# Kernel tuning notes

Hardware: AMD Instinct MI355X
Metric: run time of the kernel (lower is better)

Reference implementation:

```python
import jax, jax.numpy as jnp
import numpy as np

B, H, S, DK = 2, 16, 2048, 64

def setup_inputs() -> dict:
    key = jax.random.key(0)
    kq, kk, kv = jax.random.split(key, 3)
    shape = (B, H, S, DK)
    return {
        "multi_head_q": jax.random.normal(kq, shape, dtype=jnp.float32),
        "multi_head_k": jax.random.normal(kk, shape, dtype=jnp.float32),
        "multi_head_v": jax.random.normal(kv, shape, dtype=jnp.float32),
    }

def reference(multi_head_q, multi_head_k, multi_head_v):
    d_k = multi_head_q.shape[-1]
    scale = 1.0 / jnp.sqrt(jnp.asarray(d_k, dtype=multi_head_q.dtype))
    # scores: [B, H, S, S]
    scores = jnp.einsum("bhqd,bhkd->bhqk", multi_head_q, multi_head_k) * scale
    attn = jax.nn.softmax(scores, axis=-1)
    # z: [B, H, S, DK]
    z = jnp.einsum("bhqk,bhkd->bhqd", attn, multi_head_v)
    # transpose heads to [B, S, H, DK] then merge -> [B, S, H*DK]
    b, h, s, d = z.shape
    return jnp.swapaxes(z, 1, 2).reshape(b, s, h * d)
```

## Files before the change

kernel.cpp:

```cpp
#include <hip/hip_runtime.h>
#include <cmath>


#define S_LEN   2048
#define D_HEAD  64
#define NHEADS  16
#define NBH     32
#define TQ      128
#define TK      64
#define NTILE   (S_LEN / TK)
#define LDSTR   72
#define TILE_SH 4096

typedef short bfrag8 __attribute__((ext_vector_type(8)));
typedef float f32x4  __attribute__((ext_vector_type(4)));
typedef int   i32x2  __attribute__((ext_vector_type(2)));
typedef int   i32x4  __attribute__((ext_vector_type(4)));

static __device__ __forceinline__ short f2bf(float f) {
  unsigned int u = __builtin_bit_cast(unsigned int, f);
  u = (u + 0x7fffu + ((u >> 16) & 1u)) >> 16;
  return (short)(unsigned short)u;
}

static __device__ __forceinline__ int pk2bf(float a, float b) {
#if __has_builtin(__builtin_amdgcn_cvt_pk_bf16_f32)
  typedef __bf16 bf16x2 __attribute__((ext_vector_type(2)));
  bf16x2 r = __builtin_amdgcn_cvt_pk_bf16_f32(a, b);
  return __builtin_bit_cast(int, r);
#else
  return (int)(unsigned short)f2bf(a) | ((int)(unsigned short)f2bf(b) << 16);
#endif
}

static __device__ __forceinline__ float fexp2(float x) {
#if __has_builtin(__builtin_amdgcn_exp2f)
  return __builtin_amdgcn_exp2f(x);
#else
  return exp2f(x);
#endif
}

static __device__ __forceinline__ void gload_lds16(const short* g, short* l) {
  __builtin_amdgcn_global_load_lds(
      (const __attribute__((address_space(1))) void*)g,
      (__attribute__((address_space(3))) void*)l, 16, 0, 0);
}

__global__ __launch_bounds__(256)
void fa_prep(const float* __restrict__ K, const float* __restrict__ V,
             short* __restrict__ Kt, short* __restrict__ Vt) {
  __shared__ float fl[64][65];

  const int tid = threadIdx.x;
  const int id  = blockIdx.x;
  const int xcd = id & 7;
  const int s   = id >> 3;
  const int bh  = xcd * 4 + (s >> 5);
  const int t   = s & 31;

  const size_t ibase = ((size_t)bh * S_LEN + t * 64) * D_HEAD;
  short* kt = Kt + (size_t)(bh * NTILE + t) * TILE_SH;
  short* vt = Vt + (size_t)(bh * NTILE + t) * TILE_SH;

#pragma unroll
  for (int p = 0; p < 2; ++p) {
    int idx = p * 256 + tid;
    int key = idx >> 3, c = idx & 7;
    const float* src = K + ibase + key * 64 + c * 8;
    float4 a = *(const float4*)src;
    float4 b = *(const float4*)(src + 4);
    i32x4 w;
    w[0] = pk2bf(a.x, a.y); w[1] = pk2bf(a.z, a.w);
    w[2] = pk2bf(b.x, b.y); w[3] = pk2bf(b.z, b.w);
    *(i32x4*)(kt + key * 64 + ((c ^ (key & 7)) * 8)) = w;
  }

#pragma unroll
  for (int i = 0; i < 4; ++i) {
    int e = (i * 256 + tid) * 4;
    int row = e >> 6, col = e & 63;
    float4 v = *(const float4*)(V + ibase + (size_t)row * 64 + col);
    fl[col + 0][row] = v.x;
    fl[col + 1][row] = v.y;
    fl[col + 2][row] = v.z;
    fl[col + 3][row] = v.w;
  }
  __syncthreads();
#pragma unroll
  for (int p = 0; p < 2; ++p) {
    int idx = p * 256 + tid;
    int d = idx >> 3, ck = idx & 7;
    const float* row = &fl[d][ck * 8];
    i32x4 w;
    w[0] = pk2bf(row[0], row[1]); w[1] = pk2bf(row[2], row[3]);
    w[2] = pk2bf(row[4], row[5]); w[3] = pk2bf(row[6], row[7]);
    *(i32x4*)(vt + d * 64 + ((ck ^ (d & 7)) * 8)) = w;
  }
}

__global__ __launch_bounds__(256, 2)
void fa_fwd3(const float* __restrict__ Q, const short* __restrict__ Kt,
             const short* __restrict__ Vt, float* __restrict__ Out) {
  __shared__ short Ksb[2][TILE_SH];
  __shared__ short Vsb[2][TILE_SH];
  __shared__ short Ps [TQ * LDSTR];

  const int tid  = threadIdx.x;
  const int wid  = tid >> 6;
  const int lane = tid & 63;
  const int quad = lane >> 4;
  const int r    = lane & 15;
  const int rk   = r & 7;
  const int qb   = 32 * wid;

  const int id   = blockIdx.x;
  const int xcd  = id & 7;
  const int slot = id >> 3;
  const int bh   = xcd * 4 + (slot >> 4);
  const int q0   = (slot & 15) * TQ;

  const float qscale = 0.125f * 1.44269504088896340736f;

  const float* Qg = Q + (size_t)bh * S_LEN * D_HEAD;
  bfrag8 qf[2][2];
#pragma unroll
  for (int nt = 0; nt < 2; ++nt)
#pragma unroll
    for (int ks = 0; ks < 2; ++ks) {
      const float* qp = Qg + (size_t)(q0 + qb + 16 * nt + r) * D_HEAD + 32 * ks + 8 * quad;
      float4 a = *(const float4*)qp;
      float4 b = *(const float4*)(qp + 4);
      i32x4 w;
      w[0] = pk2bf(a.x * qscale, a.y * qscale);
      w[1] = pk2bf(a.z * qscale, a.w * qscale);
      w[2] = pk2bf(b.x * qscale, b.y * qscale);
      w[3] = pk2bf(b.z * qscale, b.w * qscale);
      qf[nt][ks] = __builtin_bit_cast(bfrag8, w);
    }

  const short* ktb = Kt + (size_t)bh * NTILE * TILE_SH;
  const short* vtb = Vt + (size_t)bh * NTILE * TILE_SH;

  auto stage = [&](int b, int t) {
    const short* ks = ktb + (size_t)t * TILE_SH;
    const short* vs = vtb + (size_t)t * TILE_SH;
#pragma unroll
    for (int n = 0; n < 2; ++n) {
      int ch = (wid * 2 + n) * 512;
      gload_lds16(ks + ch + lane * 8, &Ksb[b][ch]);
      gload_lds16(vs + ch + lane * 8, &Vsb[b][ch]);
    }
  };

  f32x4 acc[4][2];
#pragma unroll
  for (int mt = 0; mt < 4; ++mt)
#pragma unroll
    for (int nt = 0; nt < 2; ++nt)
      acc[mt][nt] = (f32x4){0.f, 0.f, 0.f, 0.f};

  float lrun[2] = {0.f, 0.f};

  auto compute = [&](const short* ksb, const short* vsb) {
    f32x4 st[4][2];
#pragma unroll
    for (int mt = 0; mt < 4; ++mt)
#pragma unroll
      for (int nt = 0; nt < 2; ++nt)
        st[mt][nt] = (f32x4){0.f, 0.f, 0.f, 0.f};

#pragma unroll
    for (int ks = 0; ks < 2; ++ks) {
      bfrag8 af[4];
#pragma unroll
      for (int mt = 0; mt < 4; ++mt)
        af[mt] = *(const bfrag8*)&ksb[(r + 16 * mt) * 64 + (((quad + 4 * ks) ^ rk) * 8)];
#pragma unroll
      for (int mt = 0; mt < 4; ++mt)
#pragma unroll
        for (int nt = 0; nt < 2; ++nt)
          st[mt][nt] = __builtin_amdgcn_mfma_f32_16x16x32_bf16(af[mt], qf[nt][ks], st[mt][nt], 0, 0, 0);
    }

#pragma unroll
    for (int nt = 0; nt < 2; ++nt) {
      float ssum = 0.f;
#pragma unroll
      for (int mt = 0; mt < 4; ++mt) {
        float p0 = fexp2(st[mt][nt][0]);
        float p1 = fexp2(st[mt][nt][1]);
        float p2 = fexp2(st[mt][nt][2]);
        float p3 = fexp2(st[mt][nt][3]);
        ssum += (p0 + p1) + (p2 + p3);
        i32x2 w;
        w[0] = pk2bf(p0, p1);
        w[1] = pk2bf(p2, p3);
        *(i32x2*)&Ps[(qb + 16 * nt + r) * LDSTR + 16 * mt + 4 * quad] = w;
      }
      lrun[nt] += ssum;
    }

#pragma unroll
    for (int ks = 0; ks < 2; ++ks) {
      bfrag8 av[4], bp[2];
#pragma unroll
      for (int mt = 0; mt < 4; ++mt)
        av[mt] = *(const bfrag8*)&vsb[(r + 16 * mt) * 64 + (((quad + 4 * ks) ^ rk) * 8)];
#pragma unroll
      for (int nt = 0; nt < 2; ++nt)
        bp[nt] = *(const bfrag8*)&Ps[(qb + 16 * nt + r) * LDSTR + quad * 8 + 32 * ks];
#pragma unroll
      for (int mt = 0; mt < 4; ++mt)
#pragma unroll
        for (int nt = 0; nt < 2; ++nt)
          acc[mt][nt] = __builtin_amdgcn_mfma_f32_16x16x32_bf16(av[mt][0] == av[mt][0] ? av[mt] : av[mt], bp[nt], acc[mt][nt], 0, 0, 0);
    }
  };

  stage(0, 0);
  for (int t = 0; t < NTILE; t += 2) {
    __syncthreads();
    stage(1, t + 1);
    compute(Ksb[0], Vsb[0]);
    __syncthreads();
    if (t + 2 < NTILE) stage(0, t + 2);
    compute(Ksb[1], Vsb[1]);
  }

  const int bb = bh >> 4, hh = bh & 15;
#pragma unroll
  for (int nt = 0; nt < 2; ++nt) {
    float l = lrun[nt];
    l += __shfl_xor(l, 16);
    l += __shfl_xor(l, 32);
    float inv = 1.0f / l;
    int qg = q0 + qb + 16 * nt + r;
    float* op = Out + ((size_t)bb * S_LEN + qg) * (NHEADS * D_HEAD) + hh * D_HEAD;
#pragma unroll
    for (int mt = 0; mt < 4; ++mt) {
      float4 o;
      o.x = acc[mt][nt][0] * inv; o.y = acc[mt][nt][1] * inv;
      o.z = acc[mt][nt][2] * inv; o.w = acc[mt][nt][3] * inv;
      *(float4*)(op + 16 * mt + 4 * quad) = o;
    }
  }
}

__global__ __launch_bounds__(256, 2)
void fa_fwd(const float* __restrict__ Q, const float* __restrict__ K,
            const float* __restrict__ V, float* __restrict__ Out) {
  __shared__ short Ks [2][TK * LDSTR];
  __shared__ short VsT[2][D_HEAD * LDSTR];
  __shared__ short Psf[TQ * LDSTR];

  const int tid  = threadIdx.x;
  const int wid  = tid >> 6;
  const int lane = tid & 63;
  const int quad = lane >> 4;
  const int r    = lane & 15;
  const int qb   = 32 * wid;

  const int bh = blockIdx.y;
  const int q0 = blockIdx.x * TQ;

  const float* Qg = Q + (size_t)bh * S_LEN * D_HEAD;
  const float* Kg = K + (size_t)bh * S_LEN * D_HEAD;
  const float* Vg = V + (size_t)bh * S_LEN * D_HEAD;

  const float qscale = 0.125f * 1.44269504088896340736f;

  bfrag8 qf[2][2];
#pragma unroll
  for (int nt = 0; nt < 2; ++nt)
#pragma unroll
    for (int ks = 0; ks < 2; ++ks) {
      const float* qp = Qg + (size_t)(q0 + qb + 16 * nt + r) * D_HEAD + 32 * ks + 8 * quad;
      float4 a = *(const float4*)qp;
      float4 b = *(const float4*)(qp + 4);
      i32x4 w;
      w[0] = pk2bf(a.x * qscale, a.y * qscale);
      w[1] = pk2bf(a.z * qscale, a.w * qscale);
      w[2] = pk2bf(b.x * qscale, b.y * qscale);
      w[3] = pk2bf(b.z * qscale, b.w * qscale);
      qf[nt][ks] = __builtin_bit_cast(bfrag8, w);
    }

  float4 kpre[4];
  float  vpre[16];

  auto load_tile = [&](int k0) {
#pragma unroll
    for (int i = 0; i < 4; ++i) {
      int e = (i * 256 + tid) * 4;
      kpre[i] = *(const float4*)(Kg + (size_t)(k0 + (e >> 6)) * D_HEAD + (e & 63));
    }
    const float* vpp = Vg + (size_t)(k0 + wid * 16) * D_HEAD + lane;
#pragma unroll
    for (int j = 0; j < 16; ++j) vpre[j] = vpp[(size_t)j * D_HEAD];
  };

  auto store_tile = [&](short* ksb, short* vsb) {
#pragma unroll
    for (int i = 0; i < 4; ++i) {
      int e = (i * 256 + tid) * 4;
      i32x2 w;
      w[0] = pk2bf(kpre[i].x, kpre[i].y);
      w[1] = pk2bf(kpre[i].z, kpre[i].w);
      *(i32x2*)&ksb[(e >> 6) * LDSTR + (e & 63)] = w;
    }
    i32x4 w0, w1;
#pragma unroll
    for (int j = 0; j < 4; ++j) w0[j] = pk2bf(vpre[2 * j],     vpre[2 * j + 1]);
#pragma unroll
    for (int j = 0; j < 4; ++j) w1[j] = pk2bf(vpre[8 + 2 * j], vpre[9 + 2 * j]);
    *(i32x4*)&vsb[lane * LDSTR + wid * 16]     = w0;
    *(i32x4*)&vsb[lane * LDSTR + wid * 16 + 8] = w1;
  };

  f32x4 acc[4][2];
#pragma unroll
  for (int mt = 0; mt < 4; ++mt)
#pragma unroll
    for (int nt = 0; nt < 2; ++nt)
      acc[mt][nt] = (f32x4){0.f, 0.f, 0.f, 0.f};

  float lrun[2] = {0.f, 0.f};

  auto compute = [&](const short* ksb, const short* vsb) {
    f32x4 st[4][2];
#pragma unroll
    for (int mt = 0; mt < 4; ++mt)
#pragma unroll
      for (int nt = 0; nt < 2; ++nt)
        st[mt][nt] = (f32x4){0.f, 0.f, 0.f, 0.f};
#pragma unroll
    for (int ks = 0; ks < 2; ++ks) {
      bfrag8 af[4];
#pragma unroll
      for (int mt = 0; mt < 4; ++mt)
        af[mt] = *(const bfrag8*)&ksb[(r + 16 * mt) * LDSTR + quad * 8 + 32 * ks];
#pragma unroll
      for (int mt = 0; mt < 4; ++mt)
#pragma unroll
        for (int nt = 0; nt < 2; ++nt)
          st[mt][nt] = __builtin_amdgcn_mfma_f32_16x16x32_bf16(af[mt], qf[nt][ks], st[mt][nt], 0, 0, 0);
    }
#pragma unroll
    for (int nt = 0; nt < 2; ++nt) {
      float ssum = 0.f;
#pragma unroll
      for (int mt = 0; mt < 4; ++mt) {
        float p0 = fexp2(st[mt][nt][0]);
        float p1 = fexp2(st[mt][nt][1]);
        float p2 = fexp2(st[mt][nt][2]);
        float p3 = fexp2(st[mt][nt][3]);
        ssum += (p0 + p1) + (p2 + p3);
        i32x2 w;
        w[0] = pk2bf(p0, p1);
        w[1] = pk2bf(p2, p3);
        *(i32x2*)&Psf[(qb + 16 * nt + r) * LDSTR + 16 * mt + 4 * quad] = w;
      }
      lrun[nt] += ssum;
    }
#pragma unroll
    for (int ks = 0; ks < 2; ++ks) {
      bfrag8 av[4], bp[2];
#pragma unroll
      for (int mt = 0; mt < 4; ++mt)
        av[mt] = *(const bfrag8*)&vsb[(r + 16 * mt) * LDSTR + quad * 8 + 32 * ks];
#pragma unroll
      for (int nt = 0; nt < 2; ++nt)
        bp[nt] = *(const bfrag8*)&Psf[(qb + 16 * nt + r) * LDSTR + quad * 8 + 32 * ks];
#pragma unroll
      for (int mt = 0; mt < 4; ++mt)
#pragma unroll
        for (int nt = 0; nt < 2; ++nt)
          acc[mt][nt] = __builtin_amdgcn_mfma_f32_16x16x32_bf16(av[mt], bp[nt], acc[mt][nt], 0, 0, 0);
    }
  };

  load_tile(0);
  store_tile(Ks[0], VsT[0]);
  load_tile(TK);

  for (int it = 0; it < NTILE; it += 2) {
    __syncthreads();
    compute(Ks[0], VsT[0]);
    store_tile(Ks[1], VsT[1]);
    if (it + 2 < NTILE) load_tile((it + 2) * TK);
    __syncthreads();
    compute(Ks[1], VsT[1]);
    if (it + 2 < NTILE) {
      store_tile(Ks[0], VsT[0]);
      if (it + 3 < NTILE) load_tile((it + 3) * TK);
    }
  }

  const int bb = bh >> 4, hh = bh & 15;
#pragma unroll
  for (int nt = 0; nt < 2; ++nt) {
    float l = lrun[nt];
    l += __shfl_xor(l, 16);
    l += __shfl_xor(l, 32);
    float inv = 1.0f / l;
    int qg = q0 + qb + 16 * nt + r;
    float* op = Out + ((size_t)bb * S_LEN + qg) * (NHEADS * D_HEAD) + hh * D_HEAD;
#pragma unroll
    for (int mt = 0; mt < 4; ++mt) {
      float4 o;
      o.x = acc[mt][nt][0] * inv; o.y = acc[mt][nt][1] * inv;
      o.z = acc[mt][nt][2] * inv; o.w = acc[mt][nt][3] * inv;
      *(float4*)(op + 16 * mt + 4 * quad) = o;
    }
  }
}

extern "C" void kernel_launch(void* const* d_in, const int* in_sizes, int n_in,
                              void* d_out, int out_size, void* d_ws, size_t ws_size,
                              hipStream_t stream) {
  const float* Q = (const float*)d_in[0];
  const float* K = (const float*)d_in[1];
  const float* V = (const float*)d_in[2];
  float* O = (float*)d_out;

  const size_t telems = (size_t)NBH * NTILE * TILE_SH;
  const size_t need   = 2 * telems * sizeof(short);

  if (ws_size >= need) {
    short* Kt = (short*)d_ws;
    short* Vt = Kt + telems;
    fa_prep<<<dim3(NBH * NTILE), 256, 0, stream>>>(K, V, Kt, Vt);
    fa_fwd3<<<dim3(512), 256, 0, stream>>>(Q, Kt, Vt, O);
  } else {
    dim3 grid(S_LEN / TQ, NBH);
    fa_fwd<<<grid, 256, 0, stream>>>(Q, K, V, O);
  }
}
```

Before: 146.5 us.

## Use 32x32x16 MFMA with register-resident P via permlane32 swap

Rewrites the attention main kernel to use 32x32x16 bf16 MFMAs, with each wave owning 32 queries and 128-thread blocks of 64 queries (1024 blocks). The P matrix is repacked in registers with v_permlane32_swap instead of going through an LDS round-trip, removing the Ps buffer and its write/read plus the LDS traffic. It adds s_setprio around the MFMA sections and splits the prep kernel into separate K and V blocks for more parallelism. The bf16 conversion helpers switch to a plain __bf16 cast. The risks are fewer waves per block to hide latency, and more K/V tile staging per block because each block now covers fewer queries.

```diff
diff --git a/kernel.cpp b/kernel.cpp
--- a/kernel.cpp
+++ b/kernel.cpp
@@ -14,23 +14,18 @@
 
 typedef short bfrag8 __attribute__((ext_vector_type(8)));
 typedef float f32x4  __attribute__((ext_vector_type(4)));
+typedef float f32x16 __attribute__((ext_vector_type(16)));
 typedef int   i32x2  __attribute__((ext_vector_type(2)));
 typedef int   i32x4  __attribute__((ext_vector_type(4)));
 
 static __device__ __forceinline__ short f2bf(float f) {
-  unsigned int u = __builtin_bit_cast(unsigned int, f);
-  u = (u + 0x7fffu + ((u >> 16) & 1u)) >> 16;
-  return (short)(unsigned short)u;
+  return (short)__builtin_bit_cast(unsigned short, (__bf16)f);
 }
 
 static __device__ __forceinline__ int pk2bf(float a, float b) {
-#if __has_builtin(__builtin_amdgcn_cvt_pk_bf16_f32)
-  typedef __bf16 bf16x2 __attribute__((ext_vector_type(2)));
-  bf16x2 r = __builtin_amdgcn_cvt_pk_bf16_f32(a, b);
-  return __builtin_bit_cast(int, r);
-#else
-  return (int)(unsigned short)f2bf(a) | ((int)(unsigned short)f2bf(b) << 16);
-#endif
+  unsigned short lo = __builtin_bit_cast(unsigned short, (__bf16)a);
+  unsigned short hi = __builtin_bit_cast(unsigned short, (__bf16)b);
+  return (int)lo | ((int)hi << 16);
 }
 
 static __device__ __forceinline__ float fexp2(float x) {
@@ -53,91 +48,92 @@
   __shared__ float fl[64][65];
 
   const int tid = threadIdx.x;
-  const int id  = blockIdx.x;
+  int id = blockIdx.x;
+  const bool isV = id >= NBH * NTILE;
+  if (isV) id -= NBH * NTILE;
   const int xcd = id & 7;
   const int s   = id >> 3;
   const int bh  = xcd * 4 + (s >> 5);
   const int t   = s & 31;
 
   const size_t ibase = ((size_t)bh * S_LEN + t * 64) * D_HEAD;
-  short* kt = Kt + (size_t)(bh * NTILE + t) * TILE_SH;
-  short* vt = Vt + (size_t)(bh * NTILE + t) * TILE_SH;
-
-#pragma unroll
-  for (int p = 0; p < 2; ++p) {
-    int idx = p * 256 + tid;
-    int key = idx >> 3, c = idx & 7;
-    const float* src = K + ibase + key * 64 + c * 8;
-    float4 a = *(const float4*)src;
-    float4 b = *(const float4*)(src + 4);
-    i32x4 w;
-    w[0] = pk2bf(a.x, a.y); w[1] = pk2bf(a.z, a.w);
-    w[2] = pk2bf(b.x, b.y); w[3] = pk2bf(b.z, b.w);
-    *(i32x4*)(kt + key * 64 + ((c ^ (key & 7)) * 8)) = w;
-  }
-
-#pragma unroll
-  for (int i = 0; i < 4; ++i) {
-    int e = (i * 256 + tid) * 4;
-    int row = e >> 6, col = e & 63;
-    float4 v = *(const float4*)(V + ibase + (size_t)row * 64 + col);
-    fl[col + 0][row] = v.x;
-    fl[col + 1][row] = v.y;
-    fl[col + 2][row] = v.z;
-    fl[col + 3][row] = v.w;
-  }
-  __syncthreads();
-#pragma unroll
-  for (int p = 0; p < 2; ++p) {
-    int idx = p * 256 + tid;
-    int d = idx >> 3, ck = idx & 7;
-    const float* row = &fl[d][ck * 8];
-    i32x4 w;
-    w[0] = pk2bf(row[0], row[1]); w[1] = pk2bf(row[2], row[3]);
-    w[2] = pk2bf(row[4], row[5]); w[3] = pk2bf(row[6], row[7]);
-    *(i32x4*)(vt + d * 64 + ((ck ^ (d & 7)) * 8)) = w;
-  }
-}
-
-__global__ __launch_bounds__(256, 2)
+
+  if (!isV) {
+    short* kt = Kt + (size_t)(bh * NTILE + t) * TILE_SH;
+#pragma unroll
+    for (int p = 0; p < 2; ++p) {
+      int idx = p * 256 + tid;
+      int key = idx >> 3, c = idx & 7;
+      const float* src = K + ibase + key * 64 + c * 8;
+      float4 a = *(const float4*)src;
+      float4 b = *(const float4*)(src + 4);
+      i32x4 w;
+      w[0] = pk2bf(a.x, a.y); w[1] = pk2bf(a.z, a.w);
+      w[2] = pk2bf(b.x, b.y); w[3] = pk2bf(b.z, b.w);
+      *(i32x4*)(kt + key * 64 + ((c ^ (key & 7)) * 8)) = w;
+    }
+  } else {
+    short* vt = Vt + (size_t)(bh * NTILE + t) * TILE_SH;
+#pragma unroll
+    for (int i = 0; i < 4; ++i) {
+      int e = (i * 256 + tid) * 4;
+      int row = e >> 6, col = e & 63;
+      float4 v = *(const float4*)(V + ibase + (size_t)row * 64 + col);
+      fl[col + 0][row] = v.x;
+      fl[col + 1][row] = v.y;
+      fl[col + 2][row] = v.z;
+      fl[col + 3][row] = v.w;
+    }
+    __syncthreads();
+#pragma unroll
+    for (int p = 0; p < 2; ++p) {
+      int idx = p * 256 + tid;
+      int d = idx >> 3, ck = idx & 7;
+      const float* row = &fl[d][ck * 8];
+      i32x4 w;
+      w[0] = pk2bf(row[0], row[1]); w[1] = pk2bf(row[2], row[3]);
+      w[2] = pk2bf(row[4], row[5]); w[3] = pk2bf(row[6], row[7]);
+      *(i32x4*)(vt + d * 64 + ((ck ^ (d & 7)) * 8)) = w;
+    }
+  }
+}
+
+__global__ __launch_bounds__(128, 2)
 void fa_fwd3(const float* __restrict__ Q, const short* __restrict__ Kt,
              const short* __restrict__ Vt, float* __restrict__ Out) {
   __shared__ short Ksb[2][TILE_SH];
   __shared__ short Vsb[2][TILE_SH];
-  __shared__ short Ps [TQ * LDSTR];
 
   const int tid  = threadIdx.x;
   const int wid  = tid >> 6;
   const int lane = tid & 63;
-  const int quad = lane >> 4;
-  const int r    = lane & 15;
-  const int rk   = r & 7;
+  const int h    = lane >> 5;
+  const int c    = lane & 31;
+  const int c7   = c & 7;
   const int qb   = 32 * wid;
 
   const int id   = blockIdx.x;
   const int xcd  = id & 7;
   const int slot = id >> 3;
-  const int bh   = xcd * 4 + (slot >> 4);
-  const int q0   = (slot & 15) * TQ;
+  const int bh   = xcd * 4 + (slot >> 5);
+  const int q0   = (slot & 31) * 64;
 
   const float qscale = 0.125f * 1.44269504088896340736f;
 
-  const float* Qg = Q + (size_t)bh * S_LEN * D_HEAD;
-  bfrag8 qf[2][2];
-#pragma unroll
-  for (int nt = 0; nt < 2; ++nt)
-#pragma unroll
-    for (int ks = 0; ks < 2; ++ks) {
-      const float* qp = Qg + (size_t)(q0 + qb + 16 * nt + r) * D_HEAD + 32 * ks + 8 * quad;
-      float4 a = *(const float4*)qp;
-      float4 b = *(const float4*)(qp + 4);
-      i32x4 w;
-      w[0] = pk2bf(a.x * qscale, a.y * qscale);
-      w[1] = pk2bf(a.z * qscale, a.w * qscale);
-      w[2] = pk2bf(b.x * qscale, b.y * qscale);
-      w[3] = pk2bf(b.z * qscale, b.w * qscale);
-      qf[nt][ks] = __builtin_bit_cast(bfrag8, w);
-    }
+  const float* Qg = Q + ((size_t)bh * S_LEN + (q0 + qb + c)) * D_HEAD;
+  bfrag8 qf[4];
+#pragma unroll
+  for (int sl = 0; sl < 4; ++sl) {
+    const float* qp = Qg + 16 * sl + 8 * h;
+    float4 a = *(const float4*)qp;
+    float4 b = *(const float4*)(qp + 4);
+    i32x4 w;
+    w[0] = pk2bf(a.x * qscale, a.y * qscale);
+    w[1] = pk2bf(a.z * qscale, a.w * qscale);
+    w[2] = pk2bf(b.x * qscale, b.y * qscale);
+    w[3] = pk2bf(b.z * qscale, b.w * qscale);
+    qf[sl] = __builtin_bit_cast(bfrag8, w);
+  }
 
   const short* ktb = Kt + (size_t)bh * NTILE * TILE_SH;
   const short* vtb = Vt + (size_t)bh * NTILE * TILE_SH;
@@ -146,76 +142,75 @@
     const short* ks = ktb + (size_t)t * TILE_SH;
     const short* vs = vtb + (size_t)t * TILE_SH;
 #pragma unroll
-    for (int n = 0; n < 2; ++n) {
-      int ch = (wid * 2 + n) * 512;
+    for (int n = 0; n < 4; ++n) {
+      int ch = (wid * 4 + n) * 512;
       gload_lds16(ks + ch + lane * 8, &Ksb[b][ch]);
       gload_lds16(vs + ch + lane * 8, &Vsb[b][ch]);
     }
   };
 
-  f32x4 acc[4][2];
-#pragma unroll
-  for (int mt = 0; mt < 4; ++mt)
-#pragma unroll
-    for (int nt = 0; nt < 2; ++nt)
-      acc[mt][nt] = (f32x4){0.f, 0.f, 0.f, 0.f};
-
-  float lrun[2] = {0.f, 0.f};
+  f32x16 acc[2];
+#pragma unroll
+  for (int m = 0; m < 2; ++m)
+#pragma unroll
+    for (int i = 0; i < 16; ++i) acc[m][i] = 0.f;
+
+  float lrun = 0.f;
 
   auto compute = [&](const short* ksb, const short* vsb) {
-    f32x4 st[4][2];
-#pragma unroll
-    for (int mt = 0; mt < 4; ++mt)
-#pragma unroll
-      for (int nt = 0; nt < 2; ++nt)
-        st[mt][nt] = (f32x4){0.f, 0.f, 0.f, 0.f};
-
-#pragma unroll
-    for (int ks = 0; ks < 2; ++ks) {
-      bfrag8 af[4];
-#pragma unroll
-      for (int mt = 0; mt < 4; ++mt)
-        af[mt] = *(const bfrag8*)&ksb[(r + 16 * mt) * 64 + (((quad + 4 * ks) ^ rk) * 8)];
-#pragma unroll
-      for (int mt = 0; mt < 4; ++mt)
-#pragma unroll
-        for (int nt = 0; nt < 2; ++nt)
-          st[mt][nt] = __builtin_amdgcn_mfma_f32_16x16x32_bf16(af[mt], qf[nt][ks], st[mt][nt], 0, 0, 0);
-    }
-
-#pragma unroll
-    for (int nt = 0; nt < 2; ++nt) {
-      float ssum = 0.f;
-#pragma unroll
-      for (int mt = 0; mt < 4; ++mt) {
-        float p0 = fexp2(st[mt][nt][0]);
-        float p1 = fexp2(st[mt][nt][1]);
-        float p2 = fexp2(st[mt][nt][2]);
-        float p3 = fexp2(st[mt][nt][3]);
-        ssum += (p0 + p1) + (p2 + p3);
-        i32x2 w;
-        w[0] = pk2bf(p0, p1);
-        w[1] = pk2bf(p2, p3);
-        *(i32x2*)&Ps[(qb + 16 * nt + r) * LDSTR + 16 * mt + 4 * quad] = w;
+    f32x16 st[2];
+#pragma unroll
+    for (int m = 0; m < 2; ++m)
+#pragma unroll
+      for (int i = 0; i < 16; ++i) st[m][i] = 0.f;
+
+    __builtin_amdgcn_s_setprio(1);
+#pragma unroll
+    for (int m2 = 0; m2 < 2; ++m2)
+#pragma unroll
+      for (int sl = 0; sl < 4; ++sl) {
+        bfrag8 af = *(const bfrag8*)
+            &ksb[(32 * m2 + c) * 64 + (((2 * sl + h) ^ c7) * 8)];
+        st[m2] = __builtin_amdgcn_mfma_f32_32x32x16_bf16(af, qf[sl], st[m2], 0, 0, 0);
       }
-      lrun[nt] += ssum;
-    }
-
-#pragma unroll
-    for (int ks = 0; ks < 2; ++ks) {
-      bfrag8 av[4], bp[2];
-#pragma unroll
-      for (int mt = 0; mt < 4; ++mt)
-        av[mt] = *(const bfrag8*)&vsb[(r + 16 * mt) * 64 + (((quad + 4 * ks) ^ rk) * 8)];
-#pragma unroll
-      for (int nt = 0; nt < 2; ++nt)
-        bp[nt] = *(const bfrag8*)&Ps[(qb + 16 * nt + r) * LDSTR + quad * 8 + 32 * ks];
-#pragma unroll
-      for (int mt = 0; mt < 4; ++mt)
-#pragma unroll
-        for (int nt = 0; nt < 2; ++nt)
-          acc[mt][nt] = __builtin_amdgcn_mfma_f32_16x16x32_bf16(av[mt][0] == av[mt][0] ? av[mt] : av[mt], bp[nt], acc[mt][nt], 0, 0, 0);
-    }
+    __builtin_amdgcn_s_setprio(0);
+
+    float ls = 0.f;
+#pragma unroll
+    for (int m2 = 0; m2 < 2; ++m2)
+#pragma unroll
+      for (int i = 0; i < 16; ++i) {
+        st[m2][i] = fexp2(st[m2][i]);
+        ls += st[m2][i];
+      }
+    lrun += ls;
+
+    bfrag8 pf[4];
+#pragma unroll
+    for (int m2 = 0; m2 < 2; ++m2)
+#pragma unroll
+      for (int hf = 0; hf < 2; ++hf) {
+        const int b0 = 8 * hf;
+        int w0 = pk2bf(st[m2][b0 + 0], st[m2][b0 + 1]);
+        int w1 = pk2bf(st[m2][b0 + 2], st[m2][b0 + 3]);
+        int w2 = pk2bf(st[m2][b0 + 4], st[m2][b0 + 5]);
+        int w3 = pk2bf(st[m2][b0 + 6], st[m2][b0 + 7]);
+        asm("v_permlane32_swap_b32 %0, %1" : "+v"(w0), "+v"(w2));
+        asm("v_permlane32_swap_b32 %0, %1" : "+v"(w1), "+v"(w3));
+        i32x4 f; f[0] = w0; f[1] = w1; f[2] = w2; f[3] = w3;
+        pf[2 * m2 + hf] = __builtin_bit_cast(bfrag8, f);
+      }
+
+    __builtin_amdgcn_s_setprio(1);
+#pragma unroll
+    for (int mtd = 0; mtd < 2; ++mtd)
+#pragma unroll
+      for (int sl = 0; sl < 4; ++sl) {
+        bfrag8 av = *(const bfrag8*)
+            &vsb[(32 * mtd + c) * 64 + (((2 * sl + h) ^ c7) * 8)];
+        acc[mtd] = __builtin_amdgcn_mfma_f32_32x32x16_bf16(av, pf[sl], acc[mtd], 0, 0, 0);
+      }
+    __builtin_amdgcn_s_setprio(0);
   };
 
   stage(0, 0);
@@ -228,23 +223,22 @@
     compute(Ksb[1], Vsb[1]);
   }
 
+  float l   = lrun + __shfl_xor(lrun, 32);
+  float inv = 1.0f / l;
   const int bb = bh >> 4, hh = bh & 15;
-#pragma unroll
-  for (int nt = 0; nt < 2; ++nt) {
-    float l = lrun[nt];
-    l += __shfl_xor(l, 16);
-    l += __shfl_xor(l, 32);
-    float inv = 1.0f / l;
-    int qg = q0 + qb + 16 * nt + r;
-    float* op = Out + ((size_t)bb * S_LEN + qg) * (NHEADS * D_HEAD) + hh * D_HEAD;
-#pragma unroll
-    for (int mt = 0; mt < 4; ++mt) {
+  const int qg = q0 + qb + c;
+  float* op = Out + ((size_t)bb * S_LEN + qg) * (NHEADS * D_HEAD) + hh * D_HEAD;
+#pragma unroll
+  for (int mtd = 0; mtd < 2; ++mtd)
+#pragma unroll
+    for (int g = 0; g < 4; ++g) {
       float4 o;
-      o.x = acc[mt][nt][0] * inv; o.y = acc[mt][nt][1] * inv;
-      o.z = acc[mt][nt][2] * inv; o.w = acc[mt][nt][3] * inv;
-      *(float4*)(op + 16 * mt + 4 * quad) = o;
-    }
-  }
+      o.x = acc[mtd][4 * g + 0] * inv;
+      o.y = acc[mtd][4 * g + 1] * inv;
+      o.z = acc[mtd][4 * g + 2] * inv;
+      o.w = acc[mtd][4 * g + 3] * inv;
+      *(float4*)(op + 32 * mtd + 8 * g + 4 * h) = o;
+    }
 }
 
 __global__ __launch_bounds__(256, 2)
@@ -430,8 +424,8 @@
   if (ws_size >= need) {
     short* Kt = (short*)d_ws;
     short* Vt = Kt + telems;
-    fa_prep<<<dim3(NBH * NTILE), 256, 0, stream>>>(K, V, Kt, Vt);
-    fa_fwd3<<<dim3(512), 256, 0, stream>>>(Q, Kt, Vt, O);
+    fa_prep<<<dim3(2 * NBH * NTILE), 256, 0, stream>>>(K, V, Kt, Vt);
+    fa_fwd3<<<dim3(1024), 128, 0, stream>>>(Q, Kt, Vt, O);
   } else {
     dim3 grid(S_LEN / TQ, NBH);
     fa_fwd<<<grid, 256, 0, stream>>>(Q, K, V, O);
```

New measurement: 141.2 us. -3.6%, faster.
